# Kernel optimization log

Hardware: AMD Instinct MI355X
Metric: run time of the kernel (lower is better)

## Reference

```python
import jax, jax.numpy as jnp
import numpy as np

EMBED_DIM = 768
NUM_HEADS = 12
HEAD_SIZE = EMBED_DIM // NUM_HEADS


def setup_inputs() -> dict:
    key = jax.random.key(0)
    ks = jax.random.split(key, 9)
    B, S, D = 4, 2048, EMBED_DIM
    scale = 1.0 / np.sqrt(D)
    x = jax.random.normal(ks[0], (B, S, D), dtype=jnp.float32)
    # Linear params (torch nn.Linear: y = x @ W.T + b); store W as [in, out] for einsum
    Wq = jax.random.normal(ks[1], (D, D), dtype=jnp.float32) * scale
    bq = jnp.zeros((D,), dtype=jnp.float32)
    Wk = jax.random.normal(ks[2], (D, D), dtype=jnp.float32) * scale
    bk = jnp.zeros((D,), dtype=jnp.float32)
    Wv = jax.random.normal(ks[3], (D, D), dtype=jnp.float32) * scale
    bv = jnp.zeros((D,), dtype=jnp.float32)
    Wo = jax.random.normal(ks[4], (D, D), dtype=jnp.float32) * scale
    bo = jnp.zeros((D,), dtype=jnp.float32)
    return {"x": x, "Wq": Wq, "bq": bq, "Wk": Wk, "bk": bk,
            "Wv": Wv, "bv": bv, "Wo": Wo, "bo": bo}


def reference(x, Wq, bq, Wk, bk, Wv, bv, Wo, bo):
    B, S, D = x.shape
    H, hs = NUM_HEADS, HEAD_SIZE
    scale = hs ** (-0.5)
    # Projections
    Q = (x @ Wq + bq).reshape(B, S, H, hs)
    K = (x @ Wk + bk).reshape(B, S, H, hs)
    V = (x @ Wv + bv).reshape(B, S, H, hs)
    # Batched attention over all heads (equivalent to the per-head loop:
    # torch view splits last dim into H contiguous chunks; concat of per-head
    # outputs along -1 restores the same layout)
    scores = jnp.einsum('bqhd,bkhd->bhqk', Q, K) * scale  # [B,H,S,S]
    attn = jax.nn.softmax(scores, axis=-1)
    out = jnp.einsum('bhqk,bkhd->bqhd', attn, V).reshape(B, S, D)
    # Output projection; dropout is identity in eval mode
    return out @ Wo + bo
```

## Files before the change

### kernel.cpp

```cpp
#include <hip/hip_runtime.h>

typedef unsigned short ushort_t;
typedef __bf16 bf16x8 __attribute__((ext_vector_type(8)));
typedef float floatx4 __attribute__((ext_vector_type(4)));

__device__ inline ushort_t f2bf(float f) {
    __bf16 h = (__bf16)f;
    return __builtin_bit_cast(ushort_t, h);
}

__device__ inline void gload16(const void* g, void* l) {
    __builtin_amdgcn_global_load_lds((const __attribute__((address_space(1))) void*)g,
                                     (__attribute__((address_space(3))) void*)l, 16, 0, 0);
}

__global__ __launch_bounds__(256) void prep_kernel(
    const float* __restrict__ x, ushort_t* __restrict__ xbf,
    const float* __restrict__ W0, const float* __restrict__ W1,
    const float* __restrict__ W2, const float* __restrict__ W3,
    ushort_t* __restrict__ T0, ushort_t* __restrict__ T1,
    ushort_t* __restrict__ T2, ushort_t* __restrict__ T3) {
    int bx = blockIdx.x;
    int tid = threadIdx.x;
    if (bx < 2304) {
        __shared__ float t[32][33];
        int w = bx / 576, rem = bx % 576;
        const float* W; ushort_t* T;
        switch (w) {
            case 0: W = W0; T = T0; break;
            case 1: W = W1; T = T1; break;
            case 2: W = W2; T = T2; break;
            default: W = W3; T = T3; break;
        }
        int n0 = (rem / 24) * 32, k0 = (rem % 24) * 32;
        int tx = tid & 31, ty = tid >> 5;
        for (int i = 0; i < 4; ++i)
            t[ty + i * 8][tx] = W[(k0 + ty + i * 8) * 768 + n0 + tx];
        __syncthreads();
        for (int i = 0; i < 4; ++i)
            T[(n0 + ty + i * 8) * 768 + k0 + tx] = f2bf(t[tx][ty + i * 8]);
    } else {
        int i = ((bx - 2304) * 256 + tid) * 4;
        float4 v = *(const float4*)(x + i);
        ushort4 u;
        u.x = f2bf(v.x); u.y = f2bf(v.y); u.z = f2bf(v.z); u.w = f2bf(v.w);
        *(ushort4*)(xbf + i) = u;
    }
}

__global__ __launch_bounds__(256) void gemm_qkv(
    const ushort_t* __restrict__ A,
    const ushort_t* __restrict__ Tq, const ushort_t* __restrict__ Tk, const ushort_t* __restrict__ Tv,
    const float* __restrict__ bq, const float* __restrict__ bk, const float* __restrict__ bv,
    ushort_t* __restrict__ Qb, ushort_t* __restrict__ Kb, ushort_t* __restrict__ Vtb) {
    __shared__ ushort_t As[128 * 64];
    __shared__ ushort_t Bs[64 * 64];
    int tid = threadIdx.x;
    int m0 = blockIdx.x * 128;
    int by = blockIdx.y;
    int which = by / 12;
    int n0 = (by % 12) * 64;
    const ushort_t* Bt = which == 0 ? Tq : (which == 1 ? Tk : Tv);
    const float* bias = which == 0 ? bq : (which == 1 ? bk : bv);

    int wave = tid >> 6;
    int lane = tid & 63;
    int ln = tid & 15;
    int quad = (tid >> 4) & 3;
    int wm = wave * 32;
    int lr = lane >> 3;
    int lc = (lane & 7) * 8;

    floatx4 acc[2][4];
    floatx4 z = {0.f, 0.f, 0.f, 0.f};
    for (int i = 0; i < 2; ++i)
        for (int j = 0; j < 4; ++j) acc[i][j] = z;

    for (int kt = 0; kt < 12; ++kt) {
        int k0 = kt * 64;
        __syncthreads();
        for (int i = 0; i < 4; ++i) {
            int c = wave * 4 + i;
            gload16(&A[(m0 + c * 8 + lr) * 768 + k0 + lc], &As[c * 512]);
        }
        for (int i = 0; i < 2; ++i) {
            int c = wave * 2 + i;
            gload16(&Bt[(n0 + c * 8 + lr) * 768 + k0 + lc], &Bs[c * 512]);
        }
        __syncthreads();
        for (int ks = 0; ks < 2; ++ks) {
            bf16x8 a[2], b[4];
            for (int i = 0; i < 2; ++i)
                a[i] = *(const bf16x8*)&As[(wm + i * 16 + ln) * 64 + ks * 32 + quad * 8];
            for (int j = 0; j < 4; ++j)
                b[j] = *(const bf16x8*)&Bs[(j * 16 + ln) * 64 + ks * 32 + quad * 8];
            for (int i = 0; i < 2; ++i)
                for (int j = 0; j < 4; ++j)
                    acc[i][j] = __builtin_amdgcn_mfma_f32_16x16x32_bf16(a[i], b[j], acc[i][j], 0, 0, 0);
        }
    }

    const float QSCALE = 0.125f * 1.44269504088896f;
    for (int i = 0; i < 2; ++i) {
        for (int j = 0; j < 4; ++j) {
            int gn = n0 + j * 16 + ln;
            float bia = bias[gn];
            int h = gn >> 6, dd = gn & 63;
            for (int r = 0; r < 4; ++r) {
                int gm = m0 + wm + i * 16 + quad * 4 + r;
                int bb = gm >> 11, ss = gm & 2047;
                float v = acc[i][j][r] + bia;
                if (which == 0) {
                    Qb[((bb * 12 + h) * 2048 + ss) * 64 + dd] = f2bf(v * QSCALE);
                } else if (which == 1) {
                    Kb[((bb * 12 + h) * 2048 + ss) * 64 + dd] = f2bf(v);
                } else {
                    Vtb[((bb * 12 + h) * 64 + dd) * 2048 + ss] = f2bf(v);
                }
            }
        }
    }
}

__global__ __launch_bounds__(256) void attn_kernel(
    const ushort_t* __restrict__ Qb, const ushort_t* __restrict__ Kb,
    const ushort_t* __restrict__ Vtb, ushort_t* __restrict__ Ob) {
    __shared__ ushort_t Ks[2][64 * 72];
    __shared__ ushort_t Vs[2][64 * 72];
    int tid = threadIdx.x;
    int qt = blockIdx.x;
    int bh = blockIdx.y;
    int wave = tid >> 6;
    int ln = tid & 15;
    int quad = (tid >> 4) & 3;
    int q0 = qt * 128 + wave * 32;

    const ushort_t* Qp = Qb + (size_t)bh * 2048 * 64;
    const ushort_t* Kp = Kb + (size_t)bh * 2048 * 64;
    const ushort_t* Vp = Vtb + (size_t)bh * 64 * 2048;

    bf16x8 bqf[2][2];
    for (int g = 0; g < 2; ++g)
        for (int ks = 0; ks < 2; ++ks)
            bqf[g][ks] = *(const bf16x8*)&Qp[(q0 + g * 16 + ln) * 64 + ks * 32 + quad * 8];

    int srow = tid >> 3;
    int c8 = tid & 7;
    int scol = c8 * 8;
    int u = c8 & 3;
    int vcol = (c8 >> 2) * 32 + (u & 1) * 16 + (u >> 1) * 4;

    uint4 kreg[2], vreg[2];

    for (int p = 0; p < 2; ++p) {
        kreg[p] = *(const uint4*)&Kp[(p * 32 + srow) * 64 + scol];
        vreg[p] = *(const uint4*)&Vp[(p * 32 + srow) * 2048 + scol];
    }
    for (int p = 0; p < 2; ++p) {
        *(uint4*)&Ks[0][(p * 32 + srow) * 72 + scol] = kreg[p];
        ushort_t* vb = &Vs[0][(p * 32 + srow) * 72 + vcol];
        *(uint2*)vb = make_uint2(vreg[p].x, vreg[p].y);
        *(uint2*)(vb + 8) = make_uint2(vreg[p].z, vreg[p].w);
    }
    __syncthreads();

    floatx4 o_acc[2][4];
    float lsum[2] = {0.f, 0.f};
    floatx4 z = {0.f, 0.f, 0.f, 0.f};
    for (int g = 0; g < 2; ++g)
        for (int m4 = 0; m4 < 4; ++m4) o_acc[g][m4] = z;

    for (int kt = 0; kt < 32; ++kt) {
        int cur = kt & 1;
        if (kt < 31) {
            for (int p = 0; p < 2; ++p) {
                kreg[p] = *(const uint4*)&Kp[((kt + 1) * 64 + p * 32 + srow) * 64 + scol];
                vreg[p] = *(const uint4*)&Vp[(p * 32 + srow) * 2048 + (kt + 1) * 64 + scol];
            }
        }

        const ushort_t* KsH = Ks[cur];
        const ushort_t* VsH = Vs[cur];

        bf16x8 ak[4][2];
        for (int m4 = 0; m4 < 4; ++m4)
            for (int ks = 0; ks < 2; ++ks)
                ak[m4][ks] = *(const bf16x8*)&KsH[(m4 * 16 + ln) * 72 + ks * 32 + quad * 8];

        floatx4 st[2][4];
        for (int g = 0; g < 2; ++g)
            for (int m4 = 0; m4 < 4; ++m4) {
                floatx4 s = z;
                s = __builtin_amdgcn_mfma_f32_16x16x32_bf16(ak[m4][0], bqf[g][0], s, 0, 0, 0);
                s = __builtin_amdgcn_mfma_f32_16x16x32_bf16(ak[m4][1], bqf[g][1], s, 0, 0, 0);
                st[g][m4] = s;
            }

        float pv[2][4][4];
        for (int g = 0; g < 2; ++g)
            for (int m4 = 0; m4 < 4; ++m4)
                for (int r = 0; r < 4; ++r) {
                    float e = __builtin_amdgcn_exp2f(st[g][m4][r]);
                    pv[g][m4][r] = e;
                    lsum[g] += e;
                }

        bf16x8 av[4][2];
        for (int m4 = 0; m4 < 4; ++m4)
            for (int c = 0; c < 2; ++c)
                av[m4][c] = *(const bf16x8*)&VsH[(m4 * 16 + ln) * 72 + c * 32 + quad * 8];

        for (int g = 0; g < 2; ++g) {
            bf16x8 bp[2];
            for (int c = 0; c < 2; ++c) {
                bf16x8 b;
                b[0] = (__bf16)pv[g][2 * c][0];
                b[1] = (__bf16)pv[g][2 * c][1];
                b[2] = (__bf16)pv[g][2 * c][2];
                b[3] = (__bf16)pv[g][2 * c][3];
                b[4] = (__bf16)pv[g][2 * c + 1][0];
                b[5] = (__bf16)pv[g][2 * c + 1][1];
                b[6] = (__bf16)pv[g][2 * c + 1][2];
                b[7] = (__bf16)pv[g][2 * c + 1][3];
                bp[c] = b;
            }
            for (int m4 = 0; m4 < 4; ++m4)
                for (int c = 0; c < 2; ++c)
                    o_acc[g][m4] = __builtin_amdgcn_mfma_f32_16x16x32_bf16(av[m4][c], bp[c], o_acc[g][m4], 0, 0, 0);
        }

        if (kt < 31) {
            int nxt = cur ^ 1;
            for (int p = 0; p < 2; ++p) {
                *(uint4*)&Ks[nxt][(p * 32 + srow) * 72 + scol] = kreg[p];
                ushort_t* vb = &Vs[nxt][(p * 32 + srow) * 72 + vcol];
                *(uint2*)vb = make_uint2(vreg[p].x, vreg[p].y);
                *(uint2*)(vb + 8) = make_uint2(vreg[p].z, vreg[p].w);
            }
        }
        __syncthreads();
    }

    for (int g = 0; g < 2; ++g) {
        lsum[g] += __shfl_xor(lsum[g], 16);
        lsum[g] += __shfl_xor(lsum[g], 32);
    }

    int b = bh / 12, h = bh % 12;
    for (int g = 0; g < 2; ++g) {
        float inv = 1.f / lsum[g];
        int token = b * 2048 + q0 + g * 16 + ln;
        for (int m4 = 0; m4 < 4; ++m4)
            for (int r = 0; r < 4; ++r)
                Ob[token * 768 + h * 64 + m4 * 16 + quad * 4 + r] = f2bf(o_acc[g][m4][r] * inv);
    }
}

__global__ __launch_bounds__(256) void gemm_out(
    const ushort_t* __restrict__ A, const ushort_t* __restrict__ Bt,
    const float* __restrict__ bias, float* __restrict__ out) {
    __shared__ ushort_t As[64 * 64];
    __shared__ ushort_t Bs[64 * 64];
    int tid = threadIdx.x;
    int m0 = blockIdx.x * 64;
    int n0 = blockIdx.y * 64;

    int wave = tid >> 6;
    int lane = tid & 63;
    int ln = tid & 15;
    int quad = (tid >> 4) & 3;
    int lr = lane >> 3;
    int lc = (lane & 7) * 8;

    floatx4 acc[4];
    floatx4 z = {0.f, 0.f, 0.f, 0.f};
    for (int i = 0; i < 4; ++i) acc[i] = z;

    for (int kt = 0; kt < 12; ++kt) {
        int k0 = kt * 64;
        __syncthreads();
        for (int i = 0; i < 2; ++i) {
            int c = wave * 2 + i;
            gload16(&A[(m0 + c * 8 + lr) * 768 + k0 + lc], &As[c * 512]);
            gload16(&Bt[(n0 + c * 8 + lr) * 768 + k0 + lc], &Bs[c * 512]);
        }
        __syncthreads();
        for (int ks = 0; ks < 2; ++ks) {
            bf16x8 b = *(const bf16x8*)&Bs[(wave * 16 + ln) * 64 + ks * 32 + quad * 8];
            for (int i = 0; i < 4; ++i) {
                bf16x8 a = *(const bf16x8*)&As[(i * 16 + ln) * 64 + ks * 32 + quad * 8];
                acc[i] = __builtin_amdgcn_mfma_f32_16x16x32_bf16(a, b, acc[i], 0, 0, 0);
            }
        }
    }

    int gn = n0 + wave * 16 + ln;
    float bia = bias[gn];
    for (int i = 0; i < 4; ++i) {
        for (int r = 0; r < 4; ++r) {
            int gm = m0 + i * 16 + quad * 4 + r;
            out[gm * 768 + gn] = acc[i][r] + bia;
        }
    }
}

extern "C" void kernel_launch(void* const* d_in, const int* in_sizes, int n_in,
                              void* d_out, int out_size, void* d_ws, size_t ws_size,
                              hipStream_t stream) {
    const float* x  = (const float*)d_in[0];
    const float* Wq = (const float*)d_in[1];
    const float* bq = (const float*)d_in[2];
    const float* Wk = (const float*)d_in[3];
    const float* bk = (const float*)d_in[4];
    const float* Wv = (const float*)d_in[5];
    const float* bv = (const float*)d_in[6];
    const float* Wo = (const float*)d_in[7];
    const float* bo = (const float*)d_in[8];

    const int NTOK = 4 * 2048;
    const int NELT = NTOK * 768;
    const int WELT = 768 * 768;

    ushort_t* xbf = (ushort_t*)d_ws;
    ushort_t* Tq  = xbf + NELT;
    ushort_t* Tk  = Tq + WELT;
    ushort_t* Tv  = Tk + WELT;
    ushort_t* To  = Tv + WELT;
    ushort_t* Qb  = To + WELT;
    ushort_t* Kb  = Qb + NELT;
    ushort_t* Vtb = Kb + NELT;
    ushort_t* Ob  = Vtb + NELT;

    prep_kernel<<<8448, 256, 0, stream>>>(x, xbf, Wq, Wk, Wv, Wo, Tq, Tk, Tv, To);
    gemm_qkv<<<dim3(64, 36), 256, 0, stream>>>(xbf, Tq, Tk, Tv, bq, bk, bv, Qb, Kb, Vtb);
    attn_kernel<<<dim3(16, 48), 256, 0, stream>>>(Qb, Kb, Vtb, Ob);
    gemm_out<<<dim3(128, 12), 256, 0, stream>>>(Ob, To, bo, (float*)d_out);
}
```

Before: 231.0 us.

## Split each KV tile across two wave groups in attention and reduce via LDS

The attention kernel now launches 512 threads per block. Two groups of four waves each process half of every 64-key tile for the same query rows, which halves the per-wave K/V fragment work and the register footprint. Partial output accumulators and row sums from the second group are written to shared memory and added by the first group before normalization and store. This raises the number of waves available to hide latency, at the cost of an extra LDS reduction and more threads taking part in each barrier.

```diff
diff --git a/kernel.cpp b/kernel.cpp
--- a/kernel.cpp
+++ b/kernel.cpp
@@ -122,18 +122,22 @@
     }
 }
 
-__global__ __launch_bounds__(256) void attn_kernel(
+__global__ __launch_bounds__(512, 6) void attn_kernel(
     const ushort_t* __restrict__ Qb, const ushort_t* __restrict__ Kb,
     const ushort_t* __restrict__ Vtb, ushort_t* __restrict__ Ob) {
-    __shared__ ushort_t Ks[2][64 * 72];
-    __shared__ ushort_t Vs[2][64 * 72];
+    __shared__ ushort_t smem[4 * 64 * 72];
+    ushort_t* KsB = smem;
+    ushort_t* VsB = smem + 2 * 64 * 72;
     int tid = threadIdx.x;
     int qt = blockIdx.x;
     int bh = blockIdx.y;
     int wave = tid >> 6;
+    int lane = tid & 63;
     int ln = tid & 15;
     int quad = (tid >> 4) & 3;
-    int q0 = qt * 128 + wave * 32;
+    int wq = wave & 3;
+    int kh = wave >> 2;
+    int q0 = qt * 128 + wq * 32;
 
     const ushort_t* Qp = Qb + (size_t)bh * 2048 * 64;
     const ushort_t* Kp = Kb + (size_t)bh * 2048 * 64;
@@ -150,17 +154,15 @@
     int u = c8 & 3;
     int vcol = (c8 >> 2) * 32 + (u & 1) * 16 + (u >> 1) * 4;
 
-    uint4 kreg[2], vreg[2];
-
-    for (int p = 0; p < 2; ++p) {
-        kreg[p] = *(const uint4*)&Kp[(p * 32 + srow) * 64 + scol];
-        vreg[p] = *(const uint4*)&Vp[(p * 32 + srow) * 2048 + scol];
-    }
-    for (int p = 0; p < 2; ++p) {
-        *(uint4*)&Ks[0][(p * 32 + srow) * 72 + scol] = kreg[p];
-        ushort_t* vb = &Vs[0][(p * 32 + srow) * 72 + vcol];
-        *(uint2*)vb = make_uint2(vreg[p].x, vreg[p].y);
-        *(uint2*)(vb + 8) = make_uint2(vreg[p].z, vreg[p].w);
+    uint4 kreg, vreg;
+
+    kreg = *(const uint4*)&Kp[srow * 64 + scol];
+    vreg = *(const uint4*)&Vp[srow * 2048 + scol];
+    *(uint4*)&KsB[srow * 72 + scol] = kreg;
+    {
+        ushort_t* vb = &VsB[srow * 72 + vcol];
+        *(uint2*)vb = make_uint2(vreg.x, vreg.y);
+        *(uint2*)(vb + 8) = make_uint2(vreg.z, vreg.w);
     }
     __syncthreads();
 
@@ -173,86 +175,92 @@
     for (int kt = 0; kt < 32; ++kt) {
         int cur = kt & 1;
         if (kt < 31) {
-            for (int p = 0; p < 2; ++p) {
-                kreg[p] = *(const uint4*)&Kp[((kt + 1) * 64 + p * 32 + srow) * 64 + scol];
-                vreg[p] = *(const uint4*)&Vp[(p * 32 + srow) * 2048 + (kt + 1) * 64 + scol];
-            }
-        }
-
-        const ushort_t* KsH = Ks[cur];
-        const ushort_t* VsH = Vs[cur];
-
-        bf16x8 ak[4][2];
-        for (int m4 = 0; m4 < 4; ++m4)
+            kreg = *(const uint4*)&Kp[((kt + 1) * 64 + srow) * 64 + scol];
+            vreg = *(const uint4*)&Vp[srow * 2048 + (kt + 1) * 64 + scol];
+        }
+
+        const ushort_t* KsH = &KsB[cur * 64 * 72];
+        const ushort_t* VsH = &VsB[cur * 64 * 72];
+
+        bf16x8 ak[2][2];
+        for (int m4 = 0; m4 < 2; ++m4)
             for (int ks = 0; ks < 2; ++ks)
-                ak[m4][ks] = *(const bf16x8*)&KsH[(m4 * 16 + ln) * 72 + ks * 32 + quad * 8];
-
-        floatx4 st[2][4];
+                ak[m4][ks] = *(const bf16x8*)&KsH[(kh * 32 + m4 * 16 + ln) * 72 + ks * 32 + quad * 8];
+
+        floatx4 st[2][2];
         for (int g = 0; g < 2; ++g)
-            for (int m4 = 0; m4 < 4; ++m4) {
+            for (int m4 = 0; m4 < 2; ++m4) {
                 floatx4 s = z;
                 s = __builtin_amdgcn_mfma_f32_16x16x32_bf16(ak[m4][0], bqf[g][0], s, 0, 0, 0);
                 s = __builtin_amdgcn_mfma_f32_16x16x32_bf16(ak[m4][1], bqf[g][1], s, 0, 0, 0);
                 st[g][m4] = s;
             }
 
-        float pv[2][4][4];
+        float pv[2][2][4];
         for (int g = 0; g < 2; ++g)
-            for (int m4 = 0; m4 < 4; ++m4)
+            for (int m4 = 0; m4 < 2; ++m4)
                 for (int r = 0; r < 4; ++r) {
                     float e = __builtin_amdgcn_exp2f(st[g][m4][r]);
                     pv[g][m4][r] = e;
                     lsum[g] += e;
                 }
 
-        bf16x8 av[4][2];
+        bf16x8 av[4];
         for (int m4 = 0; m4 < 4; ++m4)
-            for (int c = 0; c < 2; ++c)
-                av[m4][c] = *(const bf16x8*)&VsH[(m4 * 16 + ln) * 72 + c * 32 + quad * 8];
-
-        for (int g = 0; g < 2; ++g) {
-            bf16x8 bp[2];
-            for (int c = 0; c < 2; ++c) {
-                bf16x8 b;
-                b[0] = (__bf16)pv[g][2 * c][0];
-                b[1] = (__bf16)pv[g][2 * c][1];
-                b[2] = (__bf16)pv[g][2 * c][2];
-                b[3] = (__bf16)pv[g][2 * c][3];
-                b[4] = (__bf16)pv[g][2 * c + 1][0];
-                b[5] = (__bf16)pv[g][2 * c + 1][1];
-                b[6] = (__bf16)pv[g][2 * c + 1][2];
-                b[7] = (__bf16)pv[g][2 * c + 1][3];
-                bp[c] = b;
-            }
+            av[m4] = *(const bf16x8*)&VsH[(m4 * 16 + ln) * 72 + kh * 32 + quad * 8];
+
+        for (int g = 0; g < 2; ++g) {
+            bf16x8 bp;
+            bp[0] = (__bf16)pv[g][0][0];
+            bp[1] = (__bf16)pv[g][0][1];
+            bp[2] = (__bf16)pv[g][0][2];
+            bp[3] = (__bf16)pv[g][0][3];
+            bp[4] = (__bf16)pv[g][1][0];
+            bp[5] = (__bf16)pv[g][1][1];
+            bp[6] = (__bf16)pv[g][1][2];
+            bp[7] = (__bf16)pv[g][1][3];
             for (int m4 = 0; m4 < 4; ++m4)
-                for (int c = 0; c < 2; ++c)
-                    o_acc[g][m4] = __builtin_amdgcn_mfma_f32_16x16x32_bf16(av[m4][c], bp[c], o_acc[g][m4], 0, 0, 0);
+                o_acc[g][m4] = __builtin_amdgcn_mfma_f32_16x16x32_bf16(av[m4], bp, o_acc[g][m4], 0, 0, 0);
         }
 
         if (kt < 31) {
             int nxt = cur ^ 1;
-            for (int p = 0; p < 2; ++p) {
-                *(uint4*)&Ks[nxt][(p * 32 + srow) * 72 + scol] = kreg[p];
-                ushort_t* vb = &Vs[nxt][(p * 32 + srow) * 72 + vcol];
-                *(uint2*)vb = make_uint2(vreg[p].x, vreg[p].y);
-                *(uint2*)(vb + 8) = make_uint2(vreg[p].z, vreg[p].w);
-            }
-        }
-        __syncthreads();
-    }
-
-    for (int g = 0; g < 2; ++g) {
-        lsum[g] += __shfl_xor(lsum[g], 16);
-        lsum[g] += __shfl_xor(lsum[g], 32);
-    }
-
-    int b = bh / 12, h = bh % 12;
-    for (int g = 0; g < 2; ++g) {
-        float inv = 1.f / lsum[g];
-        int token = b * 2048 + q0 + g * 16 + ln;
-        for (int m4 = 0; m4 < 4; ++m4)
-            for (int r = 0; r < 4; ++r)
-                Ob[token * 768 + h * 64 + m4 * 16 + quad * 4 + r] = f2bf(o_acc[g][m4][r] * inv);
+            *(uint4*)&KsB[nxt * 64 * 72 + srow * 72 + scol] = kreg;
+            ushort_t* vb = &VsB[nxt * 64 * 72 + srow * 72 + vcol];
+            *(uint2*)vb = make_uint2(vreg.x, vreg.y);
+            *(uint2*)(vb + 8) = make_uint2(vreg.z, vreg.w);
+        }
+        __syncthreads();
+    }
+
+    floatx4* scratch = (floatx4*)smem;
+    float* lscr = (float*)(smem + 16384);
+    if (kh == 1) {
+        for (int g = 0; g < 2; ++g) {
+            for (int m4 = 0; m4 < 4; ++m4)
+                scratch[((wq * 64 + lane) * 2 + g) * 4 + m4] = o_acc[g][m4];
+            lscr[(wq * 64 + lane) * 2 + g] = lsum[g];
+        }
+    }
+    __syncthreads();
+    if (kh == 0) {
+        for (int g = 0; g < 2; ++g) {
+            for (int m4 = 0; m4 < 4; ++m4)
+                o_acc[g][m4] += scratch[((wq * 64 + lane) * 2 + g) * 4 + m4];
+            lsum[g] += lscr[(wq * 64 + lane) * 2 + g];
+        }
+        for (int g = 0; g < 2; ++g) {
+            lsum[g] += __shfl_xor(lsum[g], 16);
+            lsum[g] += __shfl_xor(lsum[g], 32);
+        }
+        int b = bh / 12, h = bh % 12;
+        for (int g = 0; g < 2; ++g) {
+            float inv = 1.f / lsum[g];
+            int token = b * 2048 + q0 + g * 16 + ln;
+            for (int m4 = 0; m4 < 4; ++m4)
+                for (int r = 0; r < 4; ++r)
+                    Ob[token * 768 + h * 64 + m4 * 16 + quad * 4 + r] = f2bf(o_acc[g][m4][r] * inv);
+        }
     }
 }
 
@@ -333,6 +341,6 @@
 
     prep_kernel<<<8448, 256, 0, stream>>>(x, xbf, Wq, Wk, Wv, Wo, Tq, Tk, Tv, To);
     gemm_qkv<<<dim3(64, 36), 256, 0, stream>>>(xbf, Tq, Tk, Tv, bq, bk, bv, Qb, Kb, Vtb);
-    attn_kernel<<<dim3(16, 48), 256, 0, stream>>>(Qb, Kb, Vtb, Ob);
+    attn_kernel<<<dim3(16, 48), 512, 0, stream>>>(Qb, Kb, Vtb, Ob);
     gemm_out<<<dim3(128, 12), 256, 0, stream>>>(Ob, To, bo, (float*)d_out);
 }
```

Result: slower. 294.8 us (+27.6%).
